# Performance work log

Hardware: AMD Instinct MI355X
Metric: run time of the kernel (lower is better)

The kernel has to match this reference:

```python
import jax, jax.numpy as jnp
import numpy as np
import math

B, H, S, D = 2, 16, 2048, 72
D12 = D // 12  # freq dim per head per component
L_PREFIX, L_SEQ = 576, 512
THETA_T = 100.0


def _make_freqs():
    n = H * D12
    log_min, log_max = math.log(math.pi), math.log(10.0 * math.pi)
    f = jnp.exp(jnp.linspace(log_min, log_max, n + 1)[:-1])  # (H*D12,)
    freqs = jnp.stack([f, f]).reshape(2, D12, H)
    freqs = jnp.swapaxes(freqs, -1, -2)  # (2, H, D12)
    t = THETA_T ** (-jnp.arange(n, dtype=jnp.float32) / n)
    t_freqs = t.reshape(D12, H).T  # (H, D12)
    return freqs.astype(jnp.float32), t_freqs.astype(jnp.float32)


def setup_inputs() -> dict:
    key = jax.random.key(0)
    ks = jax.random.split(key, 8)
    freqs, t_freqs = _make_freqs()
    return {
        "q": jax.random.normal(ks[0], (B, H, S, D), dtype=jnp.float32),
        "k": jax.random.normal(ks[1], (B, H, S, D), dtype=jnp.float32),
        "v": jax.random.normal(ks[2], (B, H, S, D), dtype=jnp.float32),
        "pos": jax.random.uniform(ks[3], (B, S, 2), dtype=jnp.float32),
        "pos_orig": jax.random.uniform(ks[4], (B, S, 2), dtype=jnp.float32),
        "time": jax.random.uniform(ks[5], (B, S), dtype=jnp.float32),
        "freqs": freqs,
        "t_freqs": t_freqs,
        "scale": jax.random.uniform(ks[6], (H, 1, 1), dtype=jnpp_f32()) if False else jax.random.uniform(ks[6], (H, 1, 1), dtype=jnp.float32) + 0.5,
        "l_prefix": L_PREFIX,
        "l_seq": L_SEQ,
    }


def jnp_f32():
    return jnp.float32


def _fp_rope_theta(pos, pos_orig, time, freqs, t_freqs):
    # FPRoPE.forward: theta per token, per head. (B,S,H,5*D12)
    p = jnp.stack([pos_orig, pos], axis=2) * 2.0 - 1.0  # (B,S,2,2)
    th_w = p[..., 0][:, :, :, None, None] * freqs[0]  # (B,S,2,H,D12)
    th_h = p[..., 1][:, :, :, None, None] * freqs[1]  # (B,S,2,H,D12)
    th_t = time[:, :, None, None, None] * t_freqs      # (B,S,1,H,D12)
    theta = jnp.concatenate([th_h, th_w, th_t], axis=2)  # (B,S,5,H,D12)
    theta = jnp.transpose(theta, (0, 3, 1, 2, 4)).reshape(B, H, S, 5 * D12)
    return theta


def _apply_rotary(x, theta):
    d = theta.shape[-1]
    x1, x2, x3 = x[..., :d], x[..., d:2 * d], x[..., 2 * d:]
    c, s = jnp.cos(theta), jnp.sin(theta)
    return jnp.concatenate([x1 * c - x2 * s, x2 * c + x1 * s, x3], axis=-1)


def _block_mask(l_prefix, l_seq):
    # inference_query_causal_mask_mod: prefix attends to nothing; pokes causal;
    # queries attend to prefix+pokes (and self via qn==kn).
    idx = jnp.arange(S)
    qn = (idx - l_prefix)[:, None]
    kn = (idx - l_prefix)[None, :]
    return (qn >= 0) & ((qn == kn) | ((qn >= kn) & (qn < l_seq)) | ((kn < l_seq) & (qn >= l_seq)))


def reference(q, k, v, pos, pos_orig, time, freqs, t_freqs, scale, l_prefix, l_seq):
    theta = _fp_rope_theta(pos, pos_orig, time, freqs, t_freqs)
    q = _apply_rotary(q, theta)
    k = _apply_rotary(k, theta)
    # cosine-similarity QK rescaling (scale_for_cosine_sim)
    eps = 1e-6
    ss = jnp.sqrt(scale)  # (H,1,1) broadcasts over (B,H,S,1)
    q = q * (ss * jax.lax.rsqrt(jnp.sum(q * q, axis=-1, keepdims=True) + eps))
    k = k * (ss * jax.lax.rsqrt(jnp.sum(k * k, axis=-1, keepdims=True) + eps))
    mask = _block_mask(l_prefix, l_seq)  # (S,S)
    scores = jnp.einsum('bhqd,bhkd->bhqk', q, k)
    scores = jnp.where(mask, scores, jnp.float32(-1e30))
    probs = jax.nn.softmax(scores, axis=-1)
    # fully-masked rows (prefix queries) output zeros, matching flex_attention
    row_valid = jnp.any(mask, axis=-1)  # (S,)
    probs = jnp.where(row_valid[None, None, :, None], probs, 0.0)
    return jnp.einsum('bhqk,bhkd->bhqd', probs, v)
```

## Files before the change

### kernel.cpp

```cpp
#include <hip/hip_runtime.h>
#include <math.h>

#define B_ 2
#define H_ 16
#define S_ 2048
#define D_ 72
#define LP 576
#define WEND 1088
#define DP 96
#define DV 80
#define NQ (S_ - LP)

#define KS 49
#define VS 17
#define PW 17
#define VBASE (32 * KS)
#define PBASE (VBASE + DV * VS)
#define LDSW (PBASE + 4 * 16 * PW)

#define NPREP2 (B_ * H_ * S_ / 8)
#define NVT    (32 * B_ * H_)

typedef __bf16 bf16x8 __attribute__((ext_vector_type(8)));
typedef float f32x4 __attribute__((ext_vector_type(4)));

static __device__ __forceinline__ unsigned pack2bf(float a, float b) {
    __bf16 x = (__bf16)a, y = (__bf16)b;
    unsigned short ux = __builtin_bit_cast(unsigned short, x);
    unsigned short uy = __builtin_bit_cast(unsigned short, y);
    return (unsigned)ux | ((unsigned)uy << 16);
}

static __device__ __forceinline__ f32x4 mfma16(bf16x8 a, bf16x8 b, f32x4 c) {
    return __builtin_amdgcn_mfma_f32_16x16x32_bf16(a, b, c, 0, 0, 0);
}

__global__ __launch_bounds__(256) void pre_kernel(
    const float* __restrict__ q, const float* __restrict__ k,
    const float* __restrict__ v,
    const float* __restrict__ pos, const float* __restrict__ pos_orig,
    const float* __restrict__ time_, const float* __restrict__ freqs,
    const float* __restrict__ t_freqs, const float* __restrict__ scale,
    unsigned* __restrict__ qn, unsigned* __restrict__ kn,
    unsigned short* __restrict__ vt, float* __restrict__ out)
{
    __shared__ __align__(16) float tile[64 * 77];
    if (blockIdx.x < NPREP2) {
        unsigned short* shp = (unsigned short*)tile;
        const int wave = threadIdx.x >> 6;
        const int lane = threadIdx.x & 63;
        const int j = lane & 31;
        const int rw = wave * 2 + (lane >> 5);
        const int row = blockIdx.x * 8 + rw;
        const int s = row & (S_ - 1);
        const int h = (row >> 11) & (H_ - 1);
        const int b = row >> 15;
        const long base = (long)row * D_;
        const int p2 = (b * S_ + s) * 2;

        float oq1 = 0.f, oq2 = 0.f, ok1 = 0.f, ok2 = 0.f;
        float pq[6], pk[6];
        float ssq = 0.f, ssk = 0.f;
        if (j < 30) {
            const float x1q = q[base + j], x2q = q[base + j + 30];
            const float x1k = k[base + j], x2k = k[base + j + 30];
            const int g = j / 6, i = j - 6 * g;
            const float fh = freqs[96 + h * 6 + i];
            const float fw = freqs[h * 6 + i];
            const float ft = t_freqs[h * 6 + i];
            const float f  = (g < 2) ? fh : ((g < 4) ? fw : ft);
            const float by_o = pos_orig[p2 + 1] * 2.f - 1.f;
            const float by_p = pos[p2 + 1]      * 2.f - 1.f;
            const float bx_o = pos_orig[p2 + 0] * 2.f - 1.f;
            const float bx_p = pos[p2 + 0]      * 2.f - 1.f;
            const float bt   = time_[b * S_ + s];
            const float bv = (g == 0) ? by_o : (g == 1) ? by_p :
                             (g == 2) ? bx_o : (g == 3) ? bx_p : bt;
            float sn, cs;
            __sincosf(bv * f, &sn, &cs);
            oq1 = x1q * cs - x2q * sn;  oq2 = x2q * cs + x1q * sn;
            ok1 = x1k * cs - x2k * sn;  ok2 = x2k * cs + x1k * sn;
            ssq = oq1 * oq1 + oq2 * oq2;
            ssk = ok1 * ok1 + ok2 * ok2;
        } else {
            const int e0 = 60 + 6 * (j - 30);
            #pragma unroll
            for (int m = 0; m < 3; ++m) {
                const float2 a = *(const float2*)(q + base + e0 + 2 * m);
                const float2 c = *(const float2*)(k + base + e0 + 2 * m);
                pq[2 * m] = a.x; pq[2 * m + 1] = a.y;
                pk[2 * m] = c.x; pk[2 * m + 1] = c.y;
                ssq += a.x * a.x + a.y * a.y;
                ssk += c.x * c.x + c.y * c.y;
            }
        }
        #pragma unroll
        for (int m = 1; m < 32; m <<= 1) { ssq += __shfl_xor(ssq, m); ssk += __shfl_xor(ssk, m); }
        const float ss = sqrtf(scale[h]);
        const float fq = ss * rsqrtf(ssq + 1e-6f);
        const float fk = ss * rsqrtf(ssk + 1e-6f);

        unsigned short* sq_ = shp + rw * 96;
        unsigned short* sk_ = shp + 768 + rw * 96;
        if (j < 30) {
            sq_[j]      = __builtin_bit_cast(unsigned short, (__bf16)(oq1 * fq));
            sq_[j + 30] = __builtin_bit_cast(unsigned short, (__bf16)(oq2 * fq));
            sk_[j]      = __builtin_bit_cast(unsigned short, (__bf16)(ok1 * fk));
            sk_[j + 30] = __builtin_bit_cast(unsigned short, (__bf16)(ok2 * fk));
        } else {
            const int e0 = 60 + 6 * (j - 30);
            #pragma unroll
            for (int m = 0; m < 6; ++m) {
                sq_[e0 + m] = __builtin_bit_cast(unsigned short, (__bf16)(pq[m] * fq));
                sk_[e0 + m] = __builtin_bit_cast(unsigned short, (__bf16)(pk[m] * fk));
            }
        }
        __syncthreads();
        const int t = threadIdx.x;
        if (t < 192) {
            const int arr = t / 96, rem = t - arr * 96;
            const int rr = rem / 12, seg = rem - rr * 12;
            uint4 val = make_uint4(0u, 0u, 0u, 0u);
            if (seg < 9) val = ((const uint4*)(shp + arr * 768 + rr * 96))[seg];
            unsigned* dst = (arr ? kn : qn) + ((long)(blockIdx.x * 8 + rr)) * 48;
            ((uint4*)dst)[seg] = val;
        }
    } else {
        const int bx2 = blockIdx.x - NPREP2;
        const int st = bx2 & 31, bh = bx2 >> 5;
        const int s0 = st * 64;
        const int t = threadIdx.x;
        if (st < 9) {
            float4* o4 = (float4*)(out + (long)(bh * S_ + s0) * D_);
            for (int i = t; i < 1152; i += 256) o4[i] = make_float4(0.f, 0.f, 0.f, 0.f);
        }
        for (int i = t; i < 1152; i += 256) {
            const int r = i / 18, c = i - r * 18;
            const float4 g = ((const float4*)v)[((long)(bh * S_ + s0 + r) * 18) + c];
            float* d = &tile[r * 77 + c * 4];
            d[0] = g.x; d[1] = g.y; d[2] = g.z; d[3] = g.w;
        }
        __syncthreads();
        for (int i = t; i < 1280; i += 256) {
            const int dd = i >> 4, s4 = i & 15;
            float f0 = 0.f, f1 = 0.f, f2 = 0.f, f3 = 0.f;
            if (dd < D_) {
                f0 = tile[(s4 * 4 + 0) * 77 + dd];
                f1 = tile[(s4 * 4 + 1) * 77 + dd];
                f2 = tile[(s4 * 4 + 2) * 77 + dd];
                f3 = tile[(s4 * 4 + 3) * 77 + dd];
            }
            uint2 o; o.x = pack2bf(f0, f1); o.y = pack2bf(f2, f3);
            ((uint2*)vt)[((((long)bh * DV + dd) << 11) + s0 + s4 * 4) >> 2] = o;
        }
    }
}

__global__ __launch_bounds__(256) void attn_kernel(
    const unsigned short* __restrict__ qn, const unsigned short* __restrict__ kn,
    const unsigned short* __restrict__ vt, float* __restrict__ out)
{
    __shared__ __align__(16) unsigned lds[LDSW];
    const int bh = blockIdx.y;
    const int q0 = LP + blockIdx.x * 64;
    const int tid = threadIdx.x;
    const int w = tid >> 6, lane = tid & 63;
    const int quad = lane >> 4, l16 = lane & 15;
    const int q0w = q0 + 16 * w;
    const bool causal = (q0 < WEND);
    const int ntiles = causal ? ((q0 + 63) >> 5) + 1 : (WEND >> 5);

    const unsigned short* qn_b = qn + (((long)bh) << 11) * DP;
    const unsigned short* kn_b = kn + (((long)bh) << 11) * DP;
    const unsigned short* vt_b = vt + (long)bh * DV * S_;

    bf16x8 qf[3];
    #pragma unroll
    for (int c = 0; c < 3; ++c)
        qf[c] = *(const bf16x8*)(qn_b + (long)(q0w + l16) * DP + c * 32 + quad * 8);

    f32x4 o[5];
    float den[4];
    #pragma unroll
    for (int dt = 0; dt < 5; ++dt) { o[dt][0]=0.f; o[dt][1]=0.f; o[dt][2]=0.f; o[dt][3]=0.f; }
    #pragma unroll
    for (int r = 0; r < 4; ++r) den[r] = 0.f;

    unsigned* Ps = lds + PBASE + w * (16 * PW);

    for (int kt = 0; kt < ntiles; ++kt) {
        const int k0 = kt * 32;
        __syncthreads();
        #pragma unroll
        for (int ii = 0; ii < 3; ++ii) {
            const int i = tid + ii * 256;
            if (i < 384) {
                const int r = i / 12, seg = i - r * 12;
                const int key = k0 + 2 * (r & 15) + (r >> 4);
                *(uint4*)(lds + r * KS + seg * 4) = *(const uint4*)(kn_b + (long)key * DP + seg * 8);
            } else if (i < 704) {
                const int j = i - 384;
                const int rr = j >> 2, seg = j & 3;
                *(uint4*)(lds + VBASE + rr * VS + seg * 4) =
                    *(const uint4*)(vt_b + (((long)rr) << 11) + k0 + seg * 8);
            }
        }
        __syncthreads();

        f32x4 acc[2];
        #pragma unroll
        for (int G = 0; G < 2; ++G) { acc[G][0]=0.f; acc[G][1]=0.f; acc[G][2]=0.f; acc[G][3]=0.f; }
        #pragma unroll
        for (int c = 0; c < 3; ++c)
            #pragma unroll
            for (int G = 0; G < 2; ++G) {
                const bf16x8 kf = *(const bf16x8*)(lds + (16 * G + l16) * KS + c * 16 + quad * 4);
                acc[G] = mfma16(qf[c], kf, acc[G]);
            }
        const int kb = k0 + 2 * l16;
        #pragma unroll
        for (int r = 0; r < 4; ++r) {
            const int qa = q0w + quad * 4 + r;
            float p0 = acc[0][r], p1 = acc[1][r];
            p0 = (!causal || kb     <= qa) ? __expf(p0) : 0.f;
            p1 = (!causal || kb + 1 <= qa) ? __expf(p1) : 0.f;
            const __bf16 pb0 = (__bf16)p0, pb1 = (__bf16)p1;
            den[r] += (float)pb0 + (float)pb1;
            Ps[(quad * 4 + r) * PW + l16] =
                (unsigned)__builtin_bit_cast(unsigned short, pb0) |
                ((unsigned)__builtin_bit_cast(unsigned short, pb1) << 16);
        }
        const bf16x8 pa = *(const bf16x8*)(Ps + l16 * PW + quad * 4);
        #pragma unroll
        for (int dt = 0; dt < 5; ++dt) {
            const bf16x8 vf = *(const bf16x8*)(lds + VBASE + (dt * 16 + l16) * VS + quad * 4);
            o[dt] = mfma16(pa, vf, o[dt]);
        }
    }

    #pragma unroll
    for (int r = 0; r < 4; ++r)
        #pragma unroll
        for (int x = 1; x < 16; x <<= 1) den[r] += __shfl_xor(den[r], x);

    if (!causal) {
        float* PsD = (float*)Ps;
        float sp = 0.f;
        #pragma unroll
        for (int c = 0; c < 3; ++c) {
            const bf16x8 kd = *(const bf16x8*)(kn_b + (long)(q0w + l16) * DP + c * 32 + quad * 8);
            #pragma unroll
            for (int j = 0; j < 8; ++j) sp += (float)qf[c][j] * (float)kd[j];
        }
        sp += __shfl_xor(sp, 16);
        sp += __shfl_xor(sp, 32);
        if (quad == 0) PsD[l16] = __expf(sp);
        #pragma unroll
        for (int r = 0; r < 4; ++r) {
            const float pd = PsD[quad * 4 + r];
            den[r] += pd;
            const int qa = q0w + quad * 4 + r;
            #pragma unroll
            for (int dt = 0; dt < 5; ++dt) {
                const unsigned short uv = vt_b[(((long)(dt * 16 + l16)) << 11) + qa];
                o[dt][r] += pd * (float)__builtin_bit_cast(__bf16, uv);
            }
        }
    }

    #pragma unroll
    for (int r = 0; r < 4; ++r) {
        const float inv = 1.f / den[r];
        const int qa = q0w + quad * 4 + r;
        float* orow = out + ((long)(bh * S_ + qa)) * D_;
        #pragma unroll
        for (int dt = 0; dt < 5; ++dt) {
            const int dim = dt * 16 + l16;
            if (dim < D_) orow[dim] = o[dt][r] * inv;
        }
    }
}

extern "C" void kernel_launch(void* const* d_in, const int* in_sizes, int n_in,
                              void* d_out, int out_size, void* d_ws, size_t ws_size,
                              hipStream_t stream) {
    const float* q        = (const float*)d_in[0];
    const float* k        = (const float*)d_in[1];
    const float* v        = (const float*)d_in[2];
    const float* pos      = (const float*)d_in[3];
    const float* pos_orig = (const float*)d_in[4];
    const float* time_    = (const float*)d_in[5];
    const float* freqs    = (const float*)d_in[6];
    const float* t_freqs  = (const float*)d_in[7];
    const float* scale    = (const float*)d_in[8];
    float* out = (float*)d_out;

    unsigned* qn = (unsigned*)d_ws;
    unsigned* kn = qn + (size_t)B_ * H_ * S_ * 48;
    unsigned short* vt = (unsigned short*)(kn + (size_t)B_ * H_ * S_ * 48);

    pre_kernel<<<dim3(NPREP2 + NVT), dim3(256), 0, stream>>>(
        q, k, v, pos, pos_orig, time_, freqs, t_freqs, scale, qn, kn, vt, out);
    attn_kernel<<<dim3(NQ / 64, B_ * H_), dim3(256), 0, stream>>>(
        (const unsigned short*)qn, (const unsigned short*)kn, vt, out);
}
```

Before: 200.5 us.

## Double-buffer K/V LDS tiles with register prefetch of next tile

Splits the K/V tile staging into a global-to-register prefetch of the next tile, issued before the current tile's MFMA work, and a later register-to-LDS write into an alternate buffer. This halves the barriers per iteration and lets global load latency overlap with compute. LDS strides change to 52/20 to fit two buffers, which raises LDS use and register pressure and may reduce occupancy or change bank-conflict behaviour.

```diff
diff --git a/kernel.cpp b/kernel.cpp
--- a/kernel.cpp
+++ b/kernel.cpp
@@ -11,12 +11,17 @@
 #define DV 80
 #define NQ (S_ - LP)
 
-#define KS 49
-#define VS 17
-#define PW 17
-#define VBASE (32 * KS)
-#define PBASE (VBASE + DV * VS)
-#define LDSW (PBASE + 4 * 16 * PW)
+#define KS 52
+#define VS 20
+#define PW 20
+#define KBUF 1664
+#define VBUF 1600
+#define K0B 0
+#define K1B KBUF
+#define V0B (2*KBUF)
+#define V1B (2*KBUF + VBUF)
+#define PBASE (2*KBUF + 2*VBUF)
+#define LDSW (PBASE + 4*16*PW)
 
 #define NPREP2 (B_ * H_ * S_ / 8)
 #define NVT    (32 * B_ * H_)
@@ -188,24 +193,53 @@
 
     unsigned* Ps = lds + PBASE + w * (16 * PW);
 
-    for (int kt = 0; kt < ntiles; ++kt) {
+    uint4 pf[3];
+
+    auto loadT = [&](int kt) {
         const int k0 = kt * 32;
-        __syncthreads();
         #pragma unroll
         for (int ii = 0; ii < 3; ++ii) {
             const int i = tid + ii * 256;
             if (i < 384) {
                 const int r = i / 12, seg = i - r * 12;
                 const int key = k0 + 2 * (r & 15) + (r >> 4);
-                *(uint4*)(lds + r * KS + seg * 4) = *(const uint4*)(kn_b + (long)key * DP + seg * 8);
+                pf[ii] = *(const uint4*)(kn_b + (long)key * DP + seg * 8);
             } else if (i < 704) {
                 const int j = i - 384;
                 const int rr = j >> 2, seg = j & 3;
-                *(uint4*)(lds + VBASE + rr * VS + seg * 4) =
-                    *(const uint4*)(vt_b + (((long)rr) << 11) + k0 + seg * 8);
-            }
-        }
-        __syncthreads();
+                pf[ii] = *(const uint4*)(vt_b + (((long)rr) << 11) + k0 + seg * 8);
+            }
+        }
+    };
+    auto writeT = [&](int b) {
+        const int kb = b ? K1B : K0B;
+        const int vb = b ? V1B : V0B;
+        #pragma unroll
+        for (int ii = 0; ii < 3; ++ii) {
+            const int i = tid + ii * 256;
+            if (i < 384) {
+                const int r = i / 12, seg = i - r * 12;
+                *(uint4*)(lds + kb + r * KS + seg * 4) = pf[ii];
+            } else if (i < 704) {
+                const int j = i - 384;
+                const int rr = j >> 2, seg = j & 3;
+                *(uint4*)(lds + vb + rr * VS + seg * 4) = pf[ii];
+            }
+        }
+    };
+
+    loadT(0);
+    writeT(0);
+    __syncthreads();
+
+    for (int kt = 0; kt < ntiles; ++kt) {
+        const int p = kt & 1;
+        const bool hasNext = (kt + 1 < ntiles);
+        if (hasNext) loadT(kt + 1);
+
+        const int kbase = p ? K1B : K0B;
+        const int vbase = p ? V1B : V0B;
+        const int k0 = kt * 32;
 
         f32x4 acc[2];
         #pragma unroll
@@ -214,16 +248,16 @@
         for (int c = 0; c < 3; ++c)
             #pragma unroll
             for (int G = 0; G < 2; ++G) {
-                const bf16x8 kf = *(const bf16x8*)(lds + (16 * G + l16) * KS + c * 16 + quad * 4);
+                const bf16x8 kf = *(const bf16x8*)(lds + kbase + (16 * G + l16) * KS + c * 16 + quad * 4);
                 acc[G] = mfma16(qf[c], kf, acc[G]);
             }
-        const int kb = k0 + 2 * l16;
+        const int kb2 = k0 + 2 * l16;
         #pragma unroll
         for (int r = 0; r < 4; ++r) {
             const int qa = q0w + quad * 4 + r;
             float p0 = acc[0][r], p1 = acc[1][r];
-            p0 = (!causal || kb     <= qa) ? __expf(p0) : 0.f;
-            p1 = (!causal || kb + 1 <= qa) ? __expf(p1) : 0.f;
+            p0 = (!causal || kb2     <= qa) ? __expf(p0) : 0.f;
+            p1 = (!causal || kb2 + 1 <= qa) ? __expf(p1) : 0.f;
             const __bf16 pb0 = (__bf16)p0, pb1 = (__bf16)p1;
             den[r] += (float)pb0 + (float)pb1;
             Ps[(quad * 4 + r) * PW + l16] =
@@ -233,9 +267,12 @@
         const bf16x8 pa = *(const bf16x8*)(Ps + l16 * PW + quad * 4);
         #pragma unroll
         for (int dt = 0; dt < 5; ++dt) {
-            const bf16x8 vf = *(const bf16x8*)(lds + VBASE + (dt * 16 + l16) * VS + quad * 4);
+            const bf16x8 vf = *(const bf16x8*)(lds + vbase + (dt * 16 + l16) * VS + quad * 4);
             o[dt] = mfma16(pa, vf, o[dt]);
         }
+
+        if (hasNext) writeT(1 - p);
+        __syncthreads();
     }
 
     #pragma unroll
```

Result: slower. 224.4 us (+11.9%).

## Split keys across waves with register-resident K/V and an LDS cross-wave reduction

Applied to the files above, without the earlier changes.

Each wave now processes all 64 queries of the block against its own 32-key slice of every 128-key tile. K and V fragments load straight from global memory into registers, which removes the per-tile LDS staging and the two block barriers per iteration. Partial outputs and denominators from the four waves are then summed through LDS before normalisation and the diagonal term. The cost is a much larger register footprint (accumulators for four query groups) and possible lower occupancy. There is also extra masked work in the last causal tile and a final reduction pass.

```diff
diff --git a/kernel.cpp b/kernel.cpp
--- a/kernel.cpp
+++ b/kernel.cpp
@@ -11,12 +11,8 @@
 #define DV 80
 #define NQ (S_ - LP)
 
-#define KS 49
-#define VS 17
-#define PW 17
-#define VBASE (32 * KS)
-#define PBASE (VBASE + DV * VS)
-#define LDSW (PBASE + 4 * 16 * PW)
+#define CBW 5376
+#define LDSW (CBW + 256 + 64)
 
 #define NPREP2 (B_ * H_ * S_ / 8)
 #define NVT    (32 * B_ * H_)
@@ -166,117 +162,154 @@
     const int tid = threadIdx.x;
     const int w = tid >> 6, lane = tid & 63;
     const int quad = lane >> 4, l16 = lane & 15;
-    const int q0w = q0 + 16 * w;
     const bool causal = (q0 < WEND);
-    const int ntiles = causal ? ((q0 + 63) >> 5) + 1 : (WEND >> 5);
+    const int ntiles = causal ? ((q0 + 191) >> 7) : 9;
 
     const unsigned short* qn_b = qn + (((long)bh) << 11) * DP;
     const unsigned short* kn_b = kn + (((long)bh) << 11) * DP;
     const unsigned short* vt_b = vt + (long)bh * DV * S_;
 
-    bf16x8 qf[3];
-    #pragma unroll
-    for (int c = 0; c < 3; ++c)
-        qf[c] = *(const bf16x8*)(qn_b + (long)(q0w + l16) * DP + c * 32 + quad * 8);
-
-    f32x4 o[5];
-    float den[4];
-    #pragma unroll
-    for (int dt = 0; dt < 5; ++dt) { o[dt][0]=0.f; o[dt][1]=0.f; o[dt][2]=0.f; o[dt][3]=0.f; }
-    #pragma unroll
-    for (int r = 0; r < 4; ++r) den[r] = 0.f;
-
-    unsigned* Ps = lds + PBASE + w * (16 * PW);
+    bf16x8 qf[4][3];
+    #pragma unroll
+    for (int m = 0; m < 4; ++m)
+        #pragma unroll
+        for (int c = 0; c < 3; ++c)
+            qf[m][c] = *(const bf16x8*)(qn_b + (long)(q0 + 16 * m + l16) * DP + c * 32 + quad * 8);
+
+    f32x4 o[4][5];
+    float den[4][4];
+    #pragma unroll
+    for (int m = 0; m < 4; ++m) {
+        #pragma unroll
+        for (int dt = 0; dt < 5; ++dt) { o[m][dt][0]=0.f; o[m][dt][1]=0.f; o[m][dt][2]=0.f; o[m][dt][3]=0.f; }
+        #pragma unroll
+        for (int r = 0; r < 4; ++r) den[m][r] = 0.f;
+    }
+
+    unsigned short* Pw = (unsigned short*)lds + w * 640;
 
     for (int kt = 0; kt < ntiles; ++kt) {
-        const int k0 = kt * 32;
+        const int kb = kt * 128 + 32 * w;
+        bf16x8 kf[2][3], vf[5];
+        #pragma unroll
+        for (int g = 0; g < 2; ++g)
+            #pragma unroll
+            for (int c = 0; c < 3; ++c)
+                kf[g][c] = *(const bf16x8*)(kn_b + (long)(kb + 16 * g + l16) * DP + c * 32 + quad * 8);
+        #pragma unroll
+        for (int dt = 0; dt < 5; ++dt)
+            vf[dt] = *(const bf16x8*)(vt_b + (((long)(dt * 16 + l16)) << 11) + kb + quad * 8);
+
+        #pragma unroll
+        for (int m = 0; m < 4; ++m) {
+            f32x4 acc0, acc1;
+            acc0[0]=0.f; acc0[1]=0.f; acc0[2]=0.f; acc0[3]=0.f;
+            acc1[0]=0.f; acc1[1]=0.f; acc1[2]=0.f; acc1[3]=0.f;
+            #pragma unroll
+            for (int c = 0; c < 3; ++c) {
+                acc0 = mfma16(qf[m][c], kf[0][c], acc0);
+                acc1 = mfma16(qf[m][c], kf[1][c], acc1);
+            }
+            #pragma unroll
+            for (int g = 0; g < 2; ++g) {
+                const int ka = kb + 16 * g + l16;
+                #pragma unroll
+                for (int r = 0; r < 4; ++r) {
+                    const int qa = q0 + 16 * m + quad * 4 + r;
+                    float p = g ? acc1[r] : acc0[r];
+                    const bool valid = causal ? (ka <= qa) : (ka < WEND);
+                    p = valid ? __expf(p) : 0.f;
+                    const __bf16 pb = (__bf16)p;
+                    den[m][r] += (float)pb;
+                    Pw[(quad * 4 + r) * 40 + 16 * g + l16] = __builtin_bit_cast(unsigned short, pb);
+                }
+            }
+            const bf16x8 pa = *(const bf16x8*)(Pw + l16 * 40 + quad * 8);
+            #pragma unroll
+            for (int dt = 0; dt < 5; ++dt)
+                o[m][dt] = mfma16(pa, vf[dt], o[m][dt]);
+        }
+    }
+
+    #pragma unroll
+    for (int m = 0; m < 4; ++m)
+        #pragma unroll
+        for (int r = 0; r < 4; ++r)
+            #pragma unroll
+            for (int x = 1; x < 16; x <<= 1) den[m][r] += __shfl_xor(den[m][r], x);
+
+    __syncthreads();
+    float* cb  = (float*)lds;
+    float* db  = (float*)lds + CBW;
+    float* PsD = (float*)lds + CBW + 256;
+    if (l16 == 0)
+        #pragma unroll
+        for (int m = 0; m < 4; ++m)
+            #pragma unroll
+            for (int r = 0; r < 4; ++r)
+                db[w * 64 + 16 * m + quad * 4 + r] = den[m][r];
+
+    float ofin[5][4];
+    #pragma unroll
+    for (int dt = 0; dt < 5; ++dt) {
         __syncthreads();
         #pragma unroll
-        for (int ii = 0; ii < 3; ++ii) {
-            const int i = tid + ii * 256;
-            if (i < 384) {
-                const int r = i / 12, seg = i - r * 12;
-                const int key = k0 + 2 * (r & 15) + (r >> 4);
-                *(uint4*)(lds + r * KS + seg * 4) = *(const uint4*)(kn_b + (long)key * DP + seg * 8);
-            } else if (i < 704) {
-                const int j = i - 384;
-                const int rr = j >> 2, seg = j & 3;
-                *(uint4*)(lds + VBASE + rr * VS + seg * 4) =
-                    *(const uint4*)(vt_b + (((long)rr) << 11) + k0 + seg * 8);
-            }
-        }
+        for (int m = 0; m < 4; ++m)
+            #pragma unroll
+            for (int r = 0; r < 4; ++r)
+                cb[w * 1344 + (16 * m + quad * 4 + r) * 21 + l16] = o[m][dt][r];
         __syncthreads();
-
-        f32x4 acc[2];
-        #pragma unroll
-        for (int G = 0; G < 2; ++G) { acc[G][0]=0.f; acc[G][1]=0.f; acc[G][2]=0.f; acc[G][3]=0.f; }
-        #pragma unroll
-        for (int c = 0; c < 3; ++c)
-            #pragma unroll
-            for (int G = 0; G < 2; ++G) {
-                const bf16x8 kf = *(const bf16x8*)(lds + (16 * G + l16) * KS + c * 16 + quad * 4);
-                acc[G] = mfma16(qf[c], kf, acc[G]);
-            }
-        const int kb = k0 + 2 * l16;
         #pragma unroll
         for (int r = 0; r < 4; ++r) {
-            const int qa = q0w + quad * 4 + r;
-            float p0 = acc[0][r], p1 = acc[1][r];
-            p0 = (!causal || kb     <= qa) ? __expf(p0) : 0.f;
-            p1 = (!causal || kb + 1 <= qa) ? __expf(p1) : 0.f;
-            const __bf16 pb0 = (__bf16)p0, pb1 = (__bf16)p1;
-            den[r] += (float)pb0 + (float)pb1;
-            Ps[(quad * 4 + r) * PW + l16] =
-                (unsigned)__builtin_bit_cast(unsigned short, pb0) |
-                ((unsigned)__builtin_bit_cast(unsigned short, pb1) << 16);
-        }
-        const bf16x8 pa = *(const bf16x8*)(Ps + l16 * PW + quad * 4);
-        #pragma unroll
-        for (int dt = 0; dt < 5; ++dt) {
-            const bf16x8 vf = *(const bf16x8*)(lds + VBASE + (dt * 16 + l16) * VS + quad * 4);
-            o[dt] = mfma16(pa, vf, o[dt]);
-        }
-    }
-
-    #pragma unroll
-    for (int r = 0; r < 4; ++r)
-        #pragma unroll
-        for (int x = 1; x < 16; x <<= 1) den[r] += __shfl_xor(den[r], x);
+            const int row = 16 * w + quad * 4 + r;
+            ofin[dt][r] = cb[row * 21 + l16] + cb[1344 + row * 21 + l16]
+                        + cb[2688 + row * 21 + l16] + cb[4032 + row * 21 + l16];
+        }
+    }
+    float dfin[4];
+    #pragma unroll
+    for (int r = 0; r < 4; ++r) {
+        const int row = 16 * w + quad * 4 + r;
+        dfin[r] = db[row] + db[64 + row] + db[128 + row] + db[192 + row];
+    }
 
     if (!causal) {
-        float* PsD = (float*)Ps;
+        bf16x8 qw[3];
+        #pragma unroll
+        for (int m = 0; m < 4; ++m)
+            if (w == m) { qw[0] = qf[m][0]; qw[1] = qf[m][1]; qw[2] = qf[m][2]; }
         float sp = 0.f;
         #pragma unroll
         for (int c = 0; c < 3; ++c) {
-            const bf16x8 kd = *(const bf16x8*)(kn_b + (long)(q0w + l16) * DP + c * 32 + quad * 8);
-            #pragma unroll
-            for (int j = 0; j < 8; ++j) sp += (float)qf[c][j] * (float)kd[j];
+            const bf16x8 kd = *(const bf16x8*)(kn_b + (long)(q0 + 16 * w + l16) * DP + c * 32 + quad * 8);
+            #pragma unroll
+            for (int j = 0; j < 8; ++j) sp += (float)qw[c][j] * (float)kd[j];
         }
         sp += __shfl_xor(sp, 16);
         sp += __shfl_xor(sp, 32);
-        if (quad == 0) PsD[l16] = __expf(sp);
+        if (quad == 0) PsD[w * 16 + l16] = __expf(sp);
         #pragma unroll
         for (int r = 0; r < 4; ++r) {
-            const float pd = PsD[quad * 4 + r];
-            den[r] += pd;
-            const int qa = q0w + quad * 4 + r;
+            const float pd = PsD[w * 16 + quad * 4 + r];
+            dfin[r] += pd;
+            const int qa = q0 + 16 * w + quad * 4 + r;
             #pragma unroll
             for (int dt = 0; dt < 5; ++dt) {
                 const unsigned short uv = vt_b[(((long)(dt * 16 + l16)) << 11) + qa];
-                o[dt][r] += pd * (float)__builtin_bit_cast(__bf16, uv);
+                ofin[dt][r] += pd * (float)__builtin_bit_cast(__bf16, uv);
             }
         }
     }
 
     #pragma unroll
     for (int r = 0; r < 4; ++r) {
-        const float inv = 1.f / den[r];
-        const int qa = q0w + quad * 4 + r;
+        const float inv = 1.f / dfin[r];
+        const int qa = q0 + 16 * w + quad * 4 + r;
         float* orow = out + ((long)(bh * S_ + qa)) * D_;
         #pragma unroll
         for (int dt = 0; dt < 5; ++dt) {
             const int dim = dt * 16 + l16;
-            if (dim < D_) orow[dim] = o[dt][r] * inv;
+            if (dim < D_) orow[dim] = ofin[dt][r] * inv;
         }
     }
 }
```

Result: faster. 178.3 us (-11.1%).
